# Optimization experiments

Measured on AMD Instinct MI355X. Metric: run time of the kernel, lower is better.

Reference implementation:

```python
import jax, jax.numpy as jnp
import numpy as np

TOPK = 8  # n_activated_experts


def setup_inputs() -> dict:
    key = jax.random.key(0)
    k1, k2 = jax.random.split(key)
    tokens, dim, n_experts = 8192, 4096, 64
    x = jax.random.normal(k1, (tokens, dim), dtype=jnp.float32)
    weight = jax.random.normal(k2, (n_experts, dim), dtype=jnp.float32) * 0.02
    bias = jnp.zeros((n_experts,), dtype=jnp.float32)
    return {"x": x, "weight": weight, "bias": bias}


def reference(x, weight, bias):
    # scores: [tokens, n_experts]
    scores = jnp.einsum("td,ed->te", x, weight) + bias
    probs = jax.nn.softmax(scores, axis=-1)  # score_func == 'softmax'
    weights, indices = jax.lax.top_k(probs, TOPK)
    return probs, indices
```

## Files before the change

### kernel.cpp

```cpp
#include <hip/hip_runtime.h>
#include <math.h>

#define NTOK    8192
#define DIM     4096
#define NEXP    64
#define TOPK_N  8
#define TAU     2.0e-4f
#define MAXFLAG 4096

#define WS_WHI_OFF  32768
#define WS_WLO_OFF  (32768 + 524288)

typedef __attribute__((ext_vector_type(8))) short short8;
typedef __attribute__((ext_vector_type(4))) float f32x4;

__device__ __forceinline__ void cvt8(float4 a0, float4 a1, short8& hv, short8& lv) {
    float f[8] = {a0.x, a0.y, a0.z, a0.w, a1.x, a1.y, a1.z, a1.w};
    union { short8 v; unsigned u[4]; } H, L;
    #pragma unroll
    for (int i = 0; i < 4; ++i) {
        unsigned b0 = __float_as_uint(f[2*i]);
        unsigned b1 = __float_as_uint(f[2*i+1]);
        float r0 = f[2*i]   - __uint_as_float(b0 & 0xffff0000u);
        float r1 = f[2*i+1] - __uint_as_float(b1 & 0xffff0000u);
        H.u[i] = (b0 >> 16) | (b1 & 0xffff0000u);
        L.u[i] = (__float_as_uint(r0) >> 16) | (__float_as_uint(r1) & 0xffff0000u);
    }
    hv = H.v; lv = L.v;
}

__global__ __launch_bounds__(256, 4)
void cvt_w_kernel(const float* __restrict__ w, unsigned short* __restrict__ whi,
                  unsigned short* __restrict__ wlo) {
    const int g = blockIdx.x * 256 + threadIdx.x;
    const float* p = w + (size_t)g * 16;
    union { short8 v; uint4 q; } H[2], L[2];
    #pragma unroll
    for (int h = 0; h < 2; ++h) {
        float4 a0 = *(const float4*)(p + h * 8);
        float4 a1 = *(const float4*)(p + h * 8 + 4);
        cvt8(a0, a1, H[h].v, L[h].v);
    }
    *(uint4*)(whi + (size_t)g * 16)     = H[0].q;
    *(uint4*)(whi + (size_t)g * 16 + 8) = H[1].q;
    *(uint4*)(wlo + (size_t)g * 16)     = L[0].q;
    *(uint4*)(wlo + (size_t)g * 16 + 8) = L[1].q;
}

__global__ __launch_bounds__(512, 2)
void gemm_kernel(const float* __restrict__ x, const unsigned short* __restrict__ whi,
                 const unsigned short* __restrict__ wlo, const float* __restrict__ bias,
                 float* __restrict__ out, int* __restrict__ flags, int ntok) {
    __shared__ float lds_acc[4 * 32 * 65];
    __shared__ float lds_s[32 * 65];

    const int tid  = threadIdx.x;
    const int lane = tid & 63;
    const int wv   = tid >> 6;
    const int mg   = wv >> 2;
    const int kq   = wv & 3;
    const int nl   = lane & 15;
    const int q    = lane >> 4;
    const int tok0 = blockIdx.x * 32;

    f32x4 acc[4];
    #pragma unroll
    for (int nf = 0; nf < 4; ++nf) acc[nf] = (f32x4){0.f, 0.f, 0.f, 0.f};

    const int kbase = kq * (DIM / 4);
    const float* xrow = x + (size_t)(tok0 + mg * 16 + nl) * DIM;

    for (int ks = 0; ks < (DIM / 4) / 32; ++ks) {
        const int k0 = kbase + ks * 32 + q * 8;
        float4 a0 = *(const float4*)(xrow + k0);
        float4 a1 = *(const float4*)(xrow + k0 + 4);
        short8 ahi, alo;
        cvt8(a0, a1, ahi, alo);
        short8 bhi[4], blo[4];
        #pragma unroll
        for (int nf = 0; nf < 4; ++nf) {
            const size_t off = (size_t)(nf * 16 + nl) * DIM + k0;
            bhi[nf] = *(const short8*)(whi + off);
            blo[nf] = *(const short8*)(wlo + off);
        }
        #pragma unroll
        for (int nf = 0; nf < 4; ++nf) {
            acc[nf] = __builtin_amdgcn_mfma_f32_16x16x32_bf16(ahi, blo[nf], acc[nf], 0, 0, 0);
            acc[nf] = __builtin_amdgcn_mfma_f32_16x16x32_bf16(alo, bhi[nf], acc[nf], 0, 0, 0);
            acc[nf] = __builtin_amdgcn_mfma_f32_16x16x32_bf16(ahi, bhi[nf], acc[nf], 0, 0, 0);
        }
    }

    #pragma unroll
    for (int nf = 0; nf < 4; ++nf)
        #pragma unroll
        for (int r = 0; r < 4; ++r) {
            const int tokl = mg * 16 + q * 4 + r;
            const int e    = nf * 16 + nl;
            lds_acc[kq * (32 * 65) + tokl * 65 + e] = acc[nf][r];
        }
    __syncthreads();

    #pragma unroll
    for (int i = 0; i < 4; ++i) {
        const int p  = tid + i * 512;
        const int tk = p >> 6, e = p & 63;
        float s = lds_acc[tk * 65 + e];
        #pragma unroll
        for (int k = 1; k < 4; ++k) s += lds_acc[k * (32 * 65) + tk * 65 + e];
        lds_s[tk * 65 + e] = s + bias[e];
    }
    __syncthreads();

    float* __restrict__ out_idx = out + (size_t)NTOK * NEXP;
    #pragma unroll
    for (int t = 0; t < 4; ++t) {
        const int tokl = wv * 4 + t;
        const int tok  = tok0 + tokl;
        const float s  = lds_s[tokl * 65 + lane];

        float m = s;
        #pragma unroll
        for (int off = 32; off > 0; off >>= 1)
            m = fmaxf(m, __shfl_xor(m, off, 64));
        const float ex = expf(s - m);
        float sum = ex;
        #pragma unroll
        for (int off = 32; off > 0; off >>= 1)
            sum += __shfl_xor(sum, off, 64);
        out[(size_t)tok * NEXP + lane] = ex / sum;

        float cv = s, prev = 0.f, ming = 1e30f;
        for (int r = 0; r < TOPK_N + 1; ++r) {
            float bv = cv;
            int   bi = lane;
            #pragma unroll
            for (int off = 32; off > 0; off >>= 1) {
                const float ov = __shfl_xor(bv, off, 64);
                const int   oi = __shfl_xor(bi, off, 64);
                if (ov > bv || (ov == bv && oi < bi)) { bv = ov; bi = oi; }
            }
            if (r > 0) ming = fminf(ming, prev - bv);
            prev = bv;
            if (r < TOPK_N && lane == r)
                out_idx[(size_t)tok * TOPK_N + r] = (float)bi;
            if (lane == bi) cv = -INFINITY;
        }
        if (lane == 0 && ming < TAU) {
            const int slot = atomicAdd(flags, 1);
            if (slot < MAXFLAG) flags[1 + slot] = tok;
        }
    }
}

__global__ __launch_bounds__(256, 2)
void recheck_kernel(const float* __restrict__ x, const float* __restrict__ w,
                    const float* __restrict__ bias, float* __restrict__ out,
                    const int* __restrict__ flags) {
    __shared__ double dsc[NEXP];
    __shared__ int    cand[NEXP + 1];
    int n = flags[0];
    if (n > MAXFLAG) n = MAXFLAG;
    const int lane = threadIdx.x & 63;
    const int wv   = threadIdx.x >> 6;
    float* __restrict__ out_idx = out + (size_t)NTOK * NEXP;

    for (int i = blockIdx.x; i < n; i += gridDim.x) {
        const int tok = flags[1 + i];
        if (wv == 0) {
            const float pe  = out[(size_t)tok * NEXP + lane];
            const int   e8  = (int)out_idx[(size_t)tok * TOPK_N + 7];
            const float thr = out[(size_t)tok * NEXP + e8] * 0.999f;
            const unsigned long long msk = __ballot(pe >= thr);
            if (lane == 0) {
                int c = 0;
                unsigned long long mm = msk;
                while (mm) { cand[1 + c++] = __builtin_ctzll(mm); mm &= mm - 1; }
                cand[0] = c;
            }
            dsc[lane] = -1.0e300;
        }
        __syncthreads();
        const int nc = cand[0];
        for (int r = wv; r < nc; r += 4) {
            const int e = cand[1 + r];
            const float* wr = w + (size_t)e * DIM;
            const float* xr = x + (size_t)tok * DIM;
            double a = 0.0;
            #pragma unroll 4
            for (int kk = 0; kk < 16; ++kk) {
                const int k = kk * 256 + lane * 4;
                const float4 wv4 = *(const float4*)(wr + k);
                const float4 xv  = *(const float4*)(xr + k);
                a = fma((double)xv.x, (double)wv4.x, a);
                a = fma((double)xv.y, (double)wv4.y, a);
                a = fma((double)xv.z, (double)wv4.z, a);
                a = fma((double)xv.w, (double)wv4.w, a);
            }
            #pragma unroll
            for (int off = 32; off > 0; off >>= 1)
                a += __shfl_xor(a, off, 64);
            if (lane == 0) dsc[e] = a + (double)bias[e];
        }
        __syncthreads();
        if (wv == 0) {
            double cv = dsc[lane];
            for (int r = 0; r < TOPK_N; ++r) {
                double bv = cv;
                int    bi = lane;
                #pragma unroll
                for (int off = 32; off > 0; off >>= 1) {
                    const double ov = __shfl_xor(bv, off, 64);
                    const int    oi = __shfl_xor(bi, off, 64);
                    if (ov > bv || (ov == bv && oi < bi)) { bv = ov; bi = oi; }
                }
                if (lane == r)
                    out_idx[(size_t)tok * TOPK_N + r] = (float)bi;
                if (lane == bi) cv = -1.0e301;
            }
        }
        __syncthreads();
    }
}

extern "C" void kernel_launch(void* const* d_in, const int* in_sizes, int n_in,
                              void* d_out, int out_size, void* d_ws, size_t ws_size,
                              hipStream_t stream) {
    const float* x  = (const float*)d_in[0];
    const float* w  = (const float*)d_in[1];
    const float* bs = (const float*)d_in[2];
    float* out = (float*)d_out;

    int* flags = (int*)d_ws;
    unsigned short* whi = (unsigned short*)((char*)d_ws + WS_WHI_OFF);
    unsigned short* wlo = (unsigned short*)((char*)d_ws + WS_WLO_OFF);

    const int ntok = in_sizes[0] / DIM;

    hipMemsetAsync(flags, 0, sizeof(int), stream);
    hipLaunchKernelGGL(cvt_w_kernel, dim3((NEXP * DIM) / 16 / 256), dim3(256), 0, stream,
                       w, whi, wlo);
    hipLaunchKernelGGL(gemm_kernel, dim3(ntok / 32), dim3(512), 0, stream,
                       x, whi, wlo, bs, out, flags, ntok);
    hipLaunchKernelGGL(recheck_kernel, dim3(256), dim3(256), 0, stream,
                       x, w, bs, out, flags);
}
```

Before: 280.9 us.

## Fuse near-tie recheck into GEMM kernel and split K across eight waves

Folds the fp64 recheck of near-tie tokens into the GEMM kernel, using shared-memory flag lists. This removes the global atomics, the memset and a separate kernel launch. Each wave now computes both 16-token halves over a K/8 slice, and loads for the next step are issued one step ahead through double-buffered registers. The candidate threshold now comes from the 9th score minus TAU rather than a probability ratio, and the block stalls while it does serial fp64 rechecks of any flagged tokens.

```diff
diff --git a/kernel.cpp b/kernel.cpp
--- a/kernel.cpp
+++ b/kernel.cpp
@@ -6,10 +6,11 @@
 #define NEXP    64
 #define TOPK_N  8
 #define TAU     2.0e-4f
-#define MAXFLAG 4096
-
-#define WS_WHI_OFF  32768
-#define WS_WLO_OFF  (32768 + 524288)
+#define KSPLIT  8
+#define KSTEPS  ((DIM / KSPLIT) / 32)
+
+#define WS_WHI_OFF  0
+#define WS_WLO_OFF  524288
 
 typedef __attribute__((ext_vector_type(8))) short short8;
 typedef __attribute__((ext_vector_type(4))) float f32x4;
@@ -50,74 +51,107 @@
 __global__ __launch_bounds__(512, 2)
 void gemm_kernel(const float* __restrict__ x, const unsigned short* __restrict__ whi,
                  const unsigned short* __restrict__ wlo, const float* __restrict__ bias,
-                 float* __restrict__ out, int* __restrict__ flags, int ntok) {
-    __shared__ float lds_acc[4 * 32 * 65];
-    __shared__ float lds_s[32 * 65];
+                 const float* __restrict__ wfp, float* __restrict__ out, int ntok) {
+    __shared__ float  lds_part[KSPLIT][32][65];
+    __shared__ float  lds_s[32][65];
+    __shared__ double dsc[NEXP];
+    __shared__ int    nflag;
+    __shared__ int    ftok[32];
+    __shared__ float  fninth[32];
 
     const int tid  = threadIdx.x;
     const int lane = tid & 63;
     const int wv   = tid >> 6;
-    const int mg   = wv >> 2;
-    const int kq   = wv & 3;
     const int nl   = lane & 15;
     const int q    = lane >> 4;
     const int tok0 = blockIdx.x * 32;
-
-    f32x4 acc[4];
-    #pragma unroll
-    for (int nf = 0; nf < 4; ++nf) acc[nf] = (f32x4){0.f, 0.f, 0.f, 0.f};
-
-    const int kbase = kq * (DIM / 4);
-    const float* xrow = x + (size_t)(tok0 + mg * 16 + nl) * DIM;
-
-    for (int ks = 0; ks < (DIM / 4) / 32; ++ks) {
-        const int k0 = kbase + ks * 32 + q * 8;
-        float4 a0 = *(const float4*)(xrow + k0);
-        float4 a1 = *(const float4*)(xrow + k0 + 4);
-        short8 ahi, alo;
-        cvt8(a0, a1, ahi, alo);
-        short8 bhi[4], blo[4];
+    if (tid == 0) nflag = 0;
+
+    const int kbase = wv * (DIM / KSPLIT);
+    const float* xr[2] = { x + (size_t)(tok0 + nl) * DIM,
+                           x + (size_t)(tok0 + 16 + nl) * DIM };
+    size_t boff[4];
+    #pragma unroll
+    for (int nf = 0; nf < 4; ++nf) boff[nf] = (size_t)(nf * 16 + nl) * DIM;
+
+    f32x4 acc[2][4];
+    #pragma unroll
+    for (int mg = 0; mg < 2; ++mg)
+        #pragma unroll
+        for (int nf = 0; nf < 4; ++nf) acc[mg][nf] = (f32x4){0.f, 0.f, 0.f, 0.f};
+
+    float4 Ar[2][2][2];
+    short8 Bh[2][4], Bl[2][4];
+
+    {
+        const int k0 = kbase + q * 8;
+        #pragma unroll
+        for (int mg = 0; mg < 2; ++mg) {
+            Ar[0][mg][0] = *(const float4*)(xr[mg] + k0);
+            Ar[0][mg][1] = *(const float4*)(xr[mg] + k0 + 4);
+        }
         #pragma unroll
         for (int nf = 0; nf < 4; ++nf) {
-            const size_t off = (size_t)(nf * 16 + nl) * DIM + k0;
-            bhi[nf] = *(const short8*)(whi + off);
-            blo[nf] = *(const short8*)(wlo + off);
-        }
-        #pragma unroll
-        for (int nf = 0; nf < 4; ++nf) {
-            acc[nf] = __builtin_amdgcn_mfma_f32_16x16x32_bf16(ahi, blo[nf], acc[nf], 0, 0, 0);
-            acc[nf] = __builtin_amdgcn_mfma_f32_16x16x32_bf16(alo, bhi[nf], acc[nf], 0, 0, 0);
-            acc[nf] = __builtin_amdgcn_mfma_f32_16x16x32_bf16(ahi, bhi[nf], acc[nf], 0, 0, 0);
-        }
-    }
-
-    #pragma unroll
-    for (int nf = 0; nf < 4; ++nf)
-        #pragma unroll
-        for (int r = 0; r < 4; ++r) {
-            const int tokl = mg * 16 + q * 4 + r;
-            const int e    = nf * 16 + nl;
-            lds_acc[kq * (32 * 65) + tokl * 65 + e] = acc[nf][r];
-        }
+            Bh[0][nf] = *(const short8*)(whi + boff[nf] + k0);
+            Bl[0][nf] = *(const short8*)(wlo + boff[nf] + k0);
+        }
+    }
+
+    #pragma unroll 2
+    for (int ks = 0; ks < KSTEPS; ++ks) {
+        const int buf = ks & 1, nxt = buf ^ 1;
+        if (ks + 1 < KSTEPS) {
+            const int k1 = kbase + (ks + 1) * 32 + q * 8;
+            #pragma unroll
+            for (int mg = 0; mg < 2; ++mg) {
+                Ar[nxt][mg][0] = *(const float4*)(xr[mg] + k1);
+                Ar[nxt][mg][1] = *(const float4*)(xr[mg] + k1 + 4);
+            }
+            #pragma unroll
+            for (int nf = 0; nf < 4; ++nf) {
+                Bh[nxt][nf] = *(const short8*)(whi + boff[nf] + k1);
+                Bl[nxt][nf] = *(const short8*)(wlo + boff[nf] + k1);
+            }
+        }
+        short8 ahi[2], alo[2];
+        cvt8(Ar[buf][0][0], Ar[buf][0][1], ahi[0], alo[0]);
+        cvt8(Ar[buf][1][0], Ar[buf][1][1], ahi[1], alo[1]);
+        #pragma unroll
+        for (int mg = 0; mg < 2; ++mg)
+            #pragma unroll
+            for (int nf = 0; nf < 4; ++nf) {
+                acc[mg][nf] = __builtin_amdgcn_mfma_f32_16x16x32_bf16(ahi[mg], Bl[buf][nf], acc[mg][nf], 0, 0, 0);
+                acc[mg][nf] = __builtin_amdgcn_mfma_f32_16x16x32_bf16(alo[mg], Bh[buf][nf], acc[mg][nf], 0, 0, 0);
+                acc[mg][nf] = __builtin_amdgcn_mfma_f32_16x16x32_bf16(ahi[mg], Bh[buf][nf], acc[mg][nf], 0, 0, 0);
+            }
+    }
+
+    #pragma unroll
+    for (int mg = 0; mg < 2; ++mg)
+        #pragma unroll
+        for (int nf = 0; nf < 4; ++nf)
+            #pragma unroll
+            for (int r = 0; r < 4; ++r)
+                lds_part[wv][mg * 16 + q * 4 + r][nf * 16 + nl] = acc[mg][nf][r];
     __syncthreads();
 
     #pragma unroll
     for (int i = 0; i < 4; ++i) {
         const int p  = tid + i * 512;
         const int tk = p >> 6, e = p & 63;
-        float s = lds_acc[tk * 65 + e];
-        #pragma unroll
-        for (int k = 1; k < 4; ++k) s += lds_acc[k * (32 * 65) + tk * 65 + e];
-        lds_s[tk * 65 + e] = s + bias[e];
+        float s = lds_part[0][tk][e];
+        #pragma unroll
+        for (int k = 1; k < KSPLIT; ++k) s += lds_part[k][tk][e];
+        lds_s[tk][e] = s + bias[e];
     }
     __syncthreads();
 
-    float* __restrict__ out_idx = out + (size_t)NTOK * NEXP;
+    float* __restrict__ out_idx = out + (size_t)ntok * NEXP;
     #pragma unroll
     for (int t = 0; t < 4; ++t) {
         const int tokl = wv * 4 + t;
         const int tok  = tok0 + tokl;
-        const float s  = lds_s[tokl * 65 + lane];
+        const float s  = lds_s[tokl][lane];
 
         float m = s;
         #pragma unroll
@@ -147,60 +181,48 @@
             if (lane == bi) cv = -INFINITY;
         }
         if (lane == 0 && ming < TAU) {
-            const int slot = atomicAdd(flags, 1);
-            if (slot < MAXFLAG) flags[1 + slot] = tok;
-        }
-    }
-}
-
-__global__ __launch_bounds__(256, 2)
-void recheck_kernel(const float* __restrict__ x, const float* __restrict__ w,
-                    const float* __restrict__ bias, float* __restrict__ out,
-                    const int* __restrict__ flags) {
-    __shared__ double dsc[NEXP];
-    __shared__ int    cand[NEXP + 1];
-    int n = flags[0];
-    if (n > MAXFLAG) n = MAXFLAG;
-    const int lane = threadIdx.x & 63;
-    const int wv   = threadIdx.x >> 6;
-    float* __restrict__ out_idx = out + (size_t)NTOK * NEXP;
-
-    for (int i = blockIdx.x; i < n; i += gridDim.x) {
-        const int tok = flags[1 + i];
-        if (wv == 0) {
-            const float pe  = out[(size_t)tok * NEXP + lane];
-            const int   e8  = (int)out_idx[(size_t)tok * TOPK_N + 7];
-            const float thr = out[(size_t)tok * NEXP + e8] * 0.999f;
-            const unsigned long long msk = __ballot(pe >= thr);
-            if (lane == 0) {
-                int c = 0;
-                unsigned long long mm = msk;
-                while (mm) { cand[1 + c++] = __builtin_ctzll(mm); mm &= mm - 1; }
-                cand[0] = c;
-            }
-            dsc[lane] = -1.0e300;
-        }
+            const int sl = atomicAdd(&nflag, 1);
+            ftok[sl] = tokl;
+            fninth[sl] = prev;
+        }
+    }
+    __syncthreads();
+
+    const int nfl = nflag;
+    for (int i = 0; i < nfl; ++i) {
+        const int tokl = ftok[i];
+        const int tok  = tok0 + tokl;
+        const float thr = fninth[i] - TAU;
+        const unsigned long long cmask = __ballot(lds_s[tokl][lane] >= thr);
+        if (wv == 0) dsc[lane] = -1.0e300;
         __syncthreads();
-        const int nc = cand[0];
-        for (int r = wv; r < nc; r += 4) {
-            const int e = cand[1 + r];
-            const float* wr = w + (size_t)e * DIM;
-            const float* xr = x + (size_t)tok * DIM;
-            double a = 0.0;
-            #pragma unroll 4
-            for (int kk = 0; kk < 16; ++kk) {
-                const int k = kk * 256 + lane * 4;
-                const float4 wv4 = *(const float4*)(wr + k);
-                const float4 xv  = *(const float4*)(xr + k);
-                a = fma((double)xv.x, (double)wv4.x, a);
-                a = fma((double)xv.y, (double)wv4.y, a);
-                a = fma((double)xv.z, (double)wv4.z, a);
-                a = fma((double)xv.w, (double)wv4.w, a);
-            }
-            #pragma unroll
-            for (int off = 32; off > 0; off >>= 1)
-                a += __shfl_xor(a, off, 64);
-            if (lane == 0) dsc[e] = a + (double)bias[e];
+        {
+            int rank = 0;
+            unsigned long long mm = cmask;
+            while (mm) {
+                const int e = __builtin_ctzll(mm);
+                mm &= mm - 1;
+                if ((rank & 7) == wv) {
+                    const float* wr = wfp + (size_t)e * DIM;
+                    const float* xrr = x + (size_t)tok * DIM;
+                    double a = 0.0;
+                    #pragma unroll 4
+                    for (int kk = 0; kk < 16; ++kk) {
+                        const int k = kk * 256 + lane * 4;
+                        const float4 wv4 = *(const float4*)(wr + k);
+                        const float4 xv  = *(const float4*)(xrr + k);
+                        a = fma((double)xv.x, (double)wv4.x, a);
+                        a = fma((double)xv.y, (double)wv4.y, a);
+                        a = fma((double)xv.z, (double)wv4.z, a);
+                        a = fma((double)xv.w, (double)wv4.w, a);
+                    }
+                    #pragma unroll
+                    for (int off = 32; off > 0; off >>= 1)
+                        a += __shfl_xor(a, off, 64);
+                    if (lane == 0) dsc[e] = a + (double)bias[e];
+                }
+                ++rank;
+            }
         }
         __syncthreads();
         if (wv == 0) {
@@ -231,17 +253,13 @@
     const float* bs = (const float*)d_in[2];
     float* out = (float*)d_out;
 
-    int* flags = (int*)d_ws;
     unsigned short* whi = (unsigned short*)((char*)d_ws + WS_WHI_OFF);
     unsigned short* wlo = (unsigned short*)((char*)d_ws + WS_WLO_OFF);
 
     const int ntok = in_sizes[0] / DIM;
 
-    hipMemsetAsync(flags, 0, sizeof(int), stream);
     hipLaunchKernelGGL(cvt_w_kernel, dim3((NEXP * DIM) / 16 / 256), dim3(256), 0, stream,
                        w, whi, wlo);
     hipLaunchKernelGGL(gemm_kernel, dim3(ntok / 32), dim3(512), 0, stream,
-                       x, whi, wlo, bs, out, flags, ntok);
-    hipLaunchKernelGGL(recheck_kernel, dim3(256), dim3(256), 0, stream,
-                       x, w, bs, out, flags);
-}
+                       x, whi, wlo, bs, w, out, ntok);
+}
```

New measurement: 255.0 us. 9.2% less time.
